# Kernel optimization log

Hardware: AMD Instinct MI355X
Metric: run time of the kernel (lower is better)

The kernel has to match this reference:

```python
import jax, jax.numpy as jnp
import numpy as np
from jax import lax

V = 33          # n_vertices
B, H, W = 8, 1024, 1024
RES = 256       # backbone input resolution
N_FEATS = 128 * 8 * 8  # 8192


def setup_inputs() -> dict:
    key = jax.random.key(0)
    ks = jax.random.split(key, 16)
    inp = {"x": jax.random.uniform(ks[0], (B, 3, H, W), jnp.float32)}
    chans = [(3, 16), (16, 32), (32, 64), (64, 128), (128, 128)]
    for i, (ci, co) in enumerate(chans):
        inp[f"cw{i}"] = jax.random.normal(ks[1 + i], (co, ci, 3, 3), jnp.float32) / float(np.sqrt(ci * 9))
        inp[f"cb{i}"] = jnp.zeros((co,), jnp.float32)
    for i, c in enumerate([16, 32, 64, 128]):
        inp[f"g{i}"] = 1.0 + 0.02 * jax.random.normal(ks[6 + i], (c,), jnp.float32)  # InstanceNorm affine init
        inp[f"be{i}"] = jnp.zeros((c,), jnp.float32)
    inp["wg_w"] = 0.01 * jax.random.normal(ks[10], (3, N_FEATS), jnp.float32)
    inp["wg_b"] = jnp.ones((3,), jnp.float32)  # init_weights: ones bias
    # basis LUT bank: rank 0 = identity LUT (meshgrid, flip(0)), other ranks small noise
    grid = jnp.stack(jnp.meshgrid(*[jnp.arange(V, dtype=jnp.float32)] * 3, indexing="ij"), 0) / (V - 1)
    identity = jnp.flip(grid, 0).reshape(1, -1)          # [1, 3*V^3]
    rest = 0.01 * jax.random.normal(ks[11], (2, 3 * V ** 3), jnp.float32)
    inp["lut_w"] = jnp.concatenate([identity, rest], 0).T  # [3*V^3, n_ranks]
    inp["vertices"] = jnp.broadcast_to(jnp.arange(V, dtype=jnp.float32) / (V - 1), (3, V))[None]  # [1,3,V]
    return inp


def _conv(x, w, b, stride=2):
    y = lax.conv_general_dilated(x, w, (stride, stride), ((1, 1), (1, 1)),
                                 dimension_numbers=("NCHW", "OIHW", "NCHW"))
    return y + b[None, :, None, None]


def _inorm(x, g, be, eps=1e-5):
    m = x.mean((2, 3), keepdims=True)
    v = x.var((2, 3), keepdims=True)  # biased, matches torch InstanceNorm
    return (x - m) / jnp.sqrt(v + eps) * g[None, :, None, None] + be[None, :, None, None]


def _leaky(x):
    return jnp.where(x >= 0, x, 0.2 * x)


def _backbone(x, cws, cbs, gs, bes):
    h = jax.image.resize(x, (x.shape[0], 3, RES, RES), "bilinear")
    for i in range(4):  # Conv -> LeakyReLU -> InstanceNorm
        h = _inorm(_leaky(_conv(h, cws[i], cbs[i])), gs[i], bes[i])
    h = _leaky(_conv(h, cws[4], cbs[4]))  # last block, no norm; dropout = identity (eval)
    return h.reshape(x.shape[0], -1)


def _ailut(img, luts, vertices):
    # img [B,3,H,W], luts [B,3,V,V,V] (axes: out_ch, b, g, r), vertices [1,3,V]
    Bn, Vn = img.shape[0], vertices.shape[-1]
    verts = jnp.broadcast_to(vertices, (Bn, 3, Vn))
    q = img.reshape(Bn * 3, -1)
    vflat = verts.reshape(Bn * 3, Vn)
    idx = jax.vmap(lambda v, qq: jnp.searchsorted(v, qq, side="right"))(vflat, q) - 1
    idx = jnp.clip(idx, 0, Vn - 2).reshape(Bn, 3, -1)       # bin index per (b, color, pixel)
    lo = jnp.take_along_axis(verts, idx, axis=2)
    hi = jnp.take_along_axis(verts, idx + 1, axis=2)
    d = (img.reshape(Bn, 3, -1) - lo) / (hi - lo)           # fractional offset
    ir, ig, ib = idx[:, 0], idx[:, 1], idx[:, 2]
    dr, dg, db = d[:, 0], d[:, 1], d[:, 2]
    lflat = luts.reshape(Bn, 3, Vn ** 3)
    out = jnp.zeros_like(d)
    for ob in (0, 1):
        for og in (0, 1):
            for orr in (0, 1):
                w = ((db if ob else 1 - db) * (dg if og else 1 - dg) * (dr if orr else 1 - dr))
                lin = ((ib + ob) * Vn + (ig + og)) * Vn + (ir + orr)
                vals = jnp.take_along_axis(lflat, lin[:, None, :], axis=2)  # [B,3,N]
                out = out + w[:, None, :] * vals
    return out.reshape(img.shape)


def reference(x, cw0, cw1, cw2, cw3, cw4, cb0, cb1, cb2, cb3, cb4,
              g0, g1, g2, g3, be0, be1, be2, be3, wg_w, wg_b, lut_w, vertices):
    codes = _backbone(x, [cw0, cw1, cw2, cw3, cw4], [cb0, cb1, cb2, cb3, cb4],
                      [g0, g1, g2, g3], [be0, be1, be2, be3])   # [B, 8192]
    weights = codes @ wg_w.T + wg_b                              # [B, 3]
    luts = (weights @ lut_w.T).reshape(x.shape[0], 3, V, V, V)   # [B,3,V,V,V]
    outs = _ailut(x, luts, vertices)
    return outs, weights, luts, vertices
```

## Files before the change

kernel.cpp:

```cpp
#include <hip/hip_runtime.h>
#include <hip/hip_bf16.h>
#include <stdint.h>

typedef unsigned int U32;

static __device__ __forceinline__ U32 f2bf_rne(float f){
  U32 u; __builtin_memcpy(&u, &f, 4);
  u = (u + 0x7fffu + ((u >> 16) & 1u)) >> 16;
  return u & 0xffffu;
}
static __device__ __forceinline__ float bflo2f(U32 p){
  U32 u = p << 16; float f; __builtin_memcpy(&f, &u, 4); return f;
}
static __device__ __forceinline__ float bfhi2f(U32 p){
  U32 u = p & 0xffff0000u; float f; __builtin_memcpy(&f, &u, 4); return f;
}

__global__ void resize_k(const float* __restrict__ x, float* __restrict__ resz){
  __shared__ float hs[68][64];
  int blk = blockIdx.x;
  int tx = blk & 3;
  int ty = (blk >> 2) & 15;
  int bc = blk >> 6;
  int ox0 = tx << 6, oy0 = ty << 4;
  int r0 = 4*oy0 - 2; if (r0 < 0) r0 = 0;
  if (r0 > 956) r0 = 958;
  const float* src = x + ((size_t)bc << 20);
  #pragma unroll 4
  for (int i = threadIdx.x; i < 68*64; i += 256){
    int r   = i >> 6;
    int oxl = i & 63;
    int ox  = ox0 + oxl;
    int rr  = r0 + r; if (rr > 1023) rr = 1023;
    const float2* row2 = (const float2*)(src + ((size_t)rr << 10));
    float acc;
    if (ox >= 1 && ox <= 254){
      float2 a = row2[2*ox-1];
      float2 b = row2[2*ox];
      float2 c = row2[2*ox+1];
      float2 d = row2[2*ox+2];
      acc = (1.f/32)*(a.x + d.y)
          + (3.f/32)*(a.y + d.x)
          + (5.f/32)*(b.x + c.y)
          + (7.f/32)*(b.y + c.x);
    } else if (ox == 0){
      float2 a = row2[0], b = row2[1], c = row2[2];
      acc = (0.625f/3.5f)*a.x + (0.875f/3.5f)*a.y
          + (0.875f/3.5f)*b.x + (0.625f/3.5f)*b.y
          + (0.375f/3.5f)*c.x + (0.125f/3.5f)*c.y;
    } else {
      float2 a = row2[509], b = row2[510], c = row2[511];
      acc = (0.125f/3.5f)*a.x + (0.375f/3.5f)*a.y
          + (0.625f/3.5f)*b.x + (0.875f/3.5f)*b.y
          + (0.875f/3.5f)*c.x + (0.625f/3.5f)*c.y;
    }
    hs[r][oxl] = acc;
  }
  __syncthreads();
  for (int i = threadIdx.x; i < 16*64; i += 256){
    int oyl = i >> 6, oxl = i & 63;
    int oy = oy0 + oyl;
    float acc;
    if (oy >= 1 && oy <= 254){
      int j0 = 4*oy - 2 - r0;
      acc = (1.f/32)*(hs[j0+0][oxl] + hs[j0+7][oxl])
          + (3.f/32)*(hs[j0+1][oxl] + hs[j0+6][oxl])
          + (5.f/32)*(hs[j0+2][oxl] + hs[j0+5][oxl])
          + (7.f/32)*(hs[j0+3][oxl] + hs[j0+4][oxl]);
    } else if (oy == 0){
      acc = (0.625f/3.5f)*hs[0][oxl] + (0.875f/3.5f)*hs[1][oxl]
          + (0.875f/3.5f)*hs[2][oxl] + (0.625f/3.5f)*hs[3][oxl]
          + (0.375f/3.5f)*hs[4][oxl] + (0.125f/3.5f)*hs[5][oxl];
    } else {
      int j0 = 1018 - r0;
      acc = (0.125f/3.5f)*hs[j0+0][oxl] + (0.375f/3.5f)*hs[j0+1][oxl]
          + (0.625f/3.5f)*hs[j0+2][oxl] + (0.875f/3.5f)*hs[j0+3][oxl]
          + (0.875f/3.5f)*hs[j0+4][oxl] + (0.625f/3.5f)*hs[j0+5][oxl];
    }
    resz[((size_t)bc << 16) + ((size_t)oy << 8) + (size_t)(ox0 + oxl)] = acc;
  }
}

__global__ void conv0_k(const float* __restrict__ in, const float* __restrict__ w,
                        const float* __restrict__ bias, float* __restrict__ out,
                        float* __restrict__ st0){
  __shared__ float tile[3][5][264];
  __shared__ float wsm[432];
  __shared__ float bs[16];
  __shared__ float sred[4][16][2];
  int t = blockIdx.x & 63;
  int b = blockIdx.x >> 6;
  for (int i = threadIdx.x; i < 432; i += 256) wsm[i] = w[i];
  if (threadIdx.x < 16) bs[threadIdx.x] = bias[threadIdx.x];
  const float* inb = in + (size_t)b*3*65536;
  int ih0 = 4*t - 1;
  for (int i = threadIdx.x; i < 3*5*258; i += 256){
    int ci  = i / (5*258);
    int rem = i % (5*258);
    int r   = rem / 258;
    int cc  = rem % 258;
    int ih  = ih0 + r;
    int iw  = cc - 1;
    float v = 0.f;
    if ((unsigned)ih < 256u && (unsigned)iw < 256u)
      v = inb[ci*65536 + ih*256 + iw];
    tile[ci][r][cc] = v;
  }
  __syncthreads();
  int lr = threadIdx.x >> 7;
  int ow = threadIdx.x & 127;
  float acc[16];
  #pragma unroll
  for (int j = 0; j < 16; j++) acc[j] = 0.f;
  #pragma unroll
  for (int ci = 0; ci < 3; ci++)
    #pragma unroll
    for (int kh = 0; kh < 3; kh++)
      #pragma unroll
      for (int kw = 0; kw < 3; kw++){
        float v = tile[ci][2*lr + kh][2*ow + kw];
        #pragma unroll
        for (int j = 0; j < 16; j++)
          acc[j] += v * wsm[j*27 + ci*9 + kh*3 + kw];
      }
  int s = t*256 + (int)threadIdx.x;
  size_t obase = (size_t)b*16*16384 + (size_t)s;
  float av[16];
  #pragma unroll
  for (int j = 0; j < 16; j++){
    float a = acc[j] + bs[j];
    a = (a >= 0.f) ? a : 0.2f*a;
    av[j] = a;
    out[obase + (size_t)j*16384] = a;
  }
  int wv = threadIdx.x >> 6;
  #pragma unroll
  for (int j = 0; j < 16; j++){
    float s1 = av[j], s2 = av[j]*av[j];
    #pragma unroll
    for (int o = 32; o > 0; o >>= 1){ s1 += __shfl_down(s1, o, 64); s2 += __shfl_down(s2, o, 64); }
    if ((threadIdx.x & 63) == 0){ sred[wv][j][0] = s1; sred[wv][j][1] = s2; }
  }
  __syncthreads();
  if (threadIdx.x < 16){
    float s1 = 0.f, s2 = 0.f;
    #pragma unroll
    for (int w2 = 0; w2 < 4; w2++){ s1 += sred[w2][threadIdx.x][0]; s2 += sred[w2][threadIdx.x][1]; }
    float* e = st0 + (((size_t)b*16 + threadIdx.x)*64 + t)*2;
    e[0] = s1; e[1] = s2;
  }
}

template<int CI, int CO, int IN, int OUT, int COB, int SPLIT, int TIN, int TOUT>
__global__ void __launch_bounds__(256, 1)
conv_leaky_k(const float* __restrict__ in, const float* __restrict__ w,
             const float* __restrict__ bias, float* __restrict__ out,
             const float* __restrict__ st_in, const float* __restrict__ g,
             const float* __restrict__ be, float* __restrict__ st_out){
  constexpr int P     = 256 / SPLIT;
  constexpr int TILES = (OUT*OUT + P - 1) / P;
  constexpr int NCB   = CO / COB;
  constexpr int CIS   = CI / SPLIT;
  constexpr int SUBS  = (TIN > 0) ? ((256/CI < TIN) ? 256/CI : TIN) : 1;
  int blk  = blockIdx.x;
  int b    = blk & 7;
  int rest = blk >> 3;
  int tile = rest % TILES;
  int cob  = rest / TILES;
  int co0  = cob * COB;
  __shared__ float ws[COB * CI * 9];
  __shared__ float bs[COB];
  __shared__ float red[(SPLIT > 1) ? 256 * COB : 1];
  __shared__ float sc[(TIN > 0) ? CI : 1];
  __shared__ float sh[(TIN > 0) ? CI : 1];
  __shared__ float pre[(TIN > 0) ? CI : 1][SUBS][2];
  for (int i = threadIdx.x; i < COB*CI*9; i += 256) ws[i] = w[(size_t)co0*CI*9 + i];
  if (threadIdx.x < COB) bs[threadIdx.x] = bias[co0 + threadIdx.x];
  if constexpr (TIN > 0){
    int c = threadIdx.x / SUBS, sub = threadIdx.x % SUBS;
    if (c < CI){
      const float* e = st_in + ((size_t)b*CI + c)*TIN*2;
      float s1 = 0.f, s2 = 0.f;
      for (int t2 = sub; t2 < TIN; t2 += SUBS){ s1 += e[t2*2]; s2 += e[t2*2+1]; }
      pre[c][sub][0] = s1; pre[c][sub][1] = s2;
    }
  }
  __syncthreads();
  if constexpr (TIN > 0){
    if (threadIdx.x < CI){
      float s1 = 0.f, s2 = 0.f;
      #pragma unroll
      for (int t2 = 0; t2 < SUBS; t2++){ s1 += pre[threadIdx.x][t2][0]; s2 += pre[threadIdx.x][t2][1]; }
      constexpr float hw = (float)(IN*IN);
      float mean = s1 * (1.f/hw);
      float var  = s2 * (1.f/hw) - mean*mean;
      float rstd = 1.f / sqrtf(var + 1e-5f);
      float scv  = g[threadIdx.x] * rstd;
      sc[threadIdx.x] = scv;
      sh[threadIdx.x] = be[threadIdx.x] - mean*scv;
    }
  }
  __syncthreads();
  int pix = threadIdx.x % P;
  int sp  = threadIdx.x / P;
  int s   = tile*P + pix;
  int oh = s / OUT, ow = s % OUT;
  float acc[COB];
  #pragma unroll
  for (int j = 0; j < COB; j++) acc[j] = 0.f;
  const float* inb = in + ((size_t)b*CI + sp*CIS) * (IN*IN);
  #pragma unroll
  for (int c0 = 0; c0 < CIS; c0 += 4){
    constexpr int CH = (CIS < 4) ? CIS : 4;
    #pragma unroll
    for (int kh = 0; kh < 3; kh++){
      int ih = oh*2 - 1 + kh;
      if ((unsigned)ih >= (unsigned)IN) continue;
      #pragma unroll
      for (int kw = 0; kw < 3; kw++){
        int iw = ow*2 - 1 + kw;
        if ((unsigned)iw >= (unsigned)IN) continue;
        const float* p0 = inb + (size_t)c0*(IN*IN) + ih*IN + iw;
        float vv[CH];
        #pragma unroll
        for (int ci = 0; ci < CH; ci++) vv[ci] = p0[(size_t)ci*(IN*IN)];
        if constexpr (TIN > 0){
          #pragma unroll
          for (int ci = 0; ci < CH; ci++) vv[ci] = vv[ci]*sc[sp*CIS+c0+ci] + sh[sp*CIS+c0+ci];
        }
        #pragma unroll
        for (int ci = 0; ci < CH; ci++){
          #pragma unroll
          for (int j = 0; j < COB; j++)
            acc[j] += vv[ci] * ws[j*CI*9 + (sp*CIS+c0+ci)*9 + kh*3 + kw];
        }
      }
    }
  }
  if constexpr (SPLIT > 1){
    #pragma unroll
    for (int j = 0; j < COB; j++) red[threadIdx.x*COB + j] = acc[j];
    __syncthreads();
    if (sp == 0){
      #pragma unroll
      for (int s2 = 1; s2 < SPLIT; s2++)
        #pragma unroll
        for (int j = 0; j < COB; j++)
          acc[j] += red[(pix + s2*P)*COB + j];
    }
  }
  float av[COB];
  if (sp == 0){
    size_t obase = ((size_t)b*CO + co0) * (size_t)(OUT*OUT) + s;
    #pragma unroll
    for (int j = 0; j < COB; j++){
      float a = acc[j] + bs[j];
      a = (a >= 0.f) ? a : 0.2f*a;
      av[j] = a;
      out[obase + (size_t)j*OUT*OUT] = a;
    }
  }
  if constexpr (TOUT > 0){
    constexpr int NW = P / 64;
    __shared__ float sred2[NW][COB][2];
    if (threadIdx.x < P){
      #pragma unroll
      for (int j = 0; j < COB; j++){
        float s1 = av[j], s2 = av[j]*av[j];
        #pragma unroll
        for (int o = 32; o > 0; o >>= 1){ s1 += __shfl_down(s1, o, 64); s2 += __shfl_down(s2, o, 64); }
        if ((threadIdx.x & 63) == 0){ int wv = threadIdx.x >> 6; sred2[wv][j][0] = s1; sred2[wv][j][1] = s2; }
      }
    }
    __syncthreads();
    if (threadIdx.x < COB){
      float s1 = 0.f, s2 = 0.f;
      #pragma unroll
      for (int wv = 0; wv < NW; wv++){ s1 += sred2[wv][threadIdx.x][0]; s2 += sred2[wv][threadIdx.x][1]; }
      float* e = st_out + (((size_t)b*CO + co0 + threadIdx.x)*TOUT + tile)*2;
      e[0] = s1; e[1] = s2;
    }
  }
}

static __device__ __forceinline__ float blockReduceSum256(float v, float* red){
  #pragma unroll
  for (int o = 32; o > 0; o >>= 1) v += __shfl_down(v, o, 64);
  __syncthreads();
  if ((threadIdx.x & 63) == 0) red[threadIdx.x >> 6] = v;
  __syncthreads();
  return red[0] + red[1] + red[2] + red[3];
}

__global__ void gemv_w_k(const float* __restrict__ codes, const float* __restrict__ wg_w,
                         const float* __restrict__ wg_b, float* __restrict__ wf,
                         float* __restrict__ outp){
  __shared__ float red[4];
  int b = blockIdx.x / 3, o = blockIdx.x % 3;
  const float* cp = codes + (size_t)b*8192;
  const float* wp = wg_w + (size_t)o*8192;
  float s = 0.f;
  for (int i = threadIdx.x; i < 8192; i += 256) s += cp[i] * wp[i];
  float tot = blockReduceSum256(s, red);
  if (threadIdx.x == 0){
    float v = tot + wg_b[o];
    wf[blockIdx.x] = v;
    outp[25165824 + blockIdx.x] = v;
  }
}

__global__ void luts_k(const float* __restrict__ wf, const float* __restrict__ lut_w,
                       const float* __restrict__ verts, U32* __restrict__ lp,
                       float* __restrict__ outp){
  int j = blockIdx.x * 256 + threadIdx.x;
  if (blockIdx.x == 0 && threadIdx.x < 99) outp[26028336 + threadIdx.x] = verts[threadIdx.x];
  if (j >= 107811) return;
  int jn = (j + 1 < 107811) ? (j + 1) : j;
  float l0 = lut_w[3*j+0], l1 = lut_w[3*j+1], l2 = lut_w[3*j+2];
  float m0 = lut_w[3*jn+0], m1 = lut_w[3*jn+1], m2 = lut_w[3*jn+2];
  int c = j / 35937;
  int i = j - c * 35937;
  #pragma unroll
  for (int b = 0; b < 8; b++){
    float w0 = wf[b*3+0], w1 = wf[b*3+1], w2 = wf[b*3+2];
    float v  = w0*l0 + w1*l1 + w2*l2;
    float vn = w0*m0 + w1*m1 + w2*m2;
    outp[25165848 + (size_t)b*107811 + j] = v;
    lp[(size_t)(b*3 + c)*35940 + i] = f2bf_rne(v) | (f2bf_rne(vn) << 16);
  }
}

static __device__ __forceinline__ void apply_phase(const U32* ls, const float4* rv,
                                                   const float4* gv, const float4* bv,
                                                   float* ob, int base){
  #pragma unroll
  for (int k = 0; k < 4; k++){
    float rr[4] = {rv[k].x, rv[k].y, rv[k].z, rv[k].w};
    float gg[4] = {gv[k].x, gv[k].y, gv[k].z, gv[k].w};
    float bb[4] = {bv[k].x, bv[k].y, bv[k].z, bv[k].w};
    U32 pw[4][4];
    float w00[4], w01[4], w10[4], w11[4], drx[4];
    #pragma unroll
    for (int h = 0; h < 4; h++){
      float rq = rr[h] * 32.f;
      float gq = gg[h] * 32.f;
      float bq = bb[h] * 32.f;
      int ir = (int)rq; ir = ir > 31 ? 31 : ir;
      int ig = (int)gq; ig = ig > 31 ? 31 : ig;
      int ib = (int)bq; ib = ib > 31 ? 31 : ib;
      float dr = rq - (float)ir;
      float dg = gq - (float)ig;
      float db = bq - (float)ib;
      int lin = (ib*33 + ig)*33 + ir;
      pw[h][0] = ls[lin];
      pw[h][1] = ls[lin+33];
      pw[h][2] = ls[lin+1089];
      pw[h][3] = ls[lin+1122];
      float t = db*dg;
      w11[h] = t;
      w10[h] = db - t;
      w01[h] = dg - t;
      w00[h] = 1.f - db - dg + t;
      drx[h] = dr;
    }
    float res[4];
    #pragma unroll
    for (int h = 0; h < 4; h++){
      float odr = 1.f - drx[h];
      float v0 = odr*bflo2f(pw[h][0]) + drx[h]*bfhi2f(pw[h][0]);
      float v1 = odr*bflo2f(pw[h][1]) + drx[h]*bfhi2f(pw[h][1]);
      float v2 = odr*bflo2f(pw[h][2]) + drx[h]*bfhi2f(pw[h][2]);
      float v3 = odr*bflo2f(pw[h][3]) + drx[h]*bfhi2f(pw[h][3]);
      res[h] = w00[h]*v0 + w01[h]*v1 + w10[h]*v2 + w11[h]*v3;
    }
    *(float4*)(ob + base + k*4096) = make_float4(res[0], res[1], res[2], res[3]);
  }
}

__global__ void __launch_bounds__(1024, 4) ailut_apply_k(const float* __restrict__ x,
                                                         const U32* __restrict__ lp,
                                                         float* __restrict__ outp){
  __shared__ U32 ls[35936];
  int b = blockIdx.z, c = blockIdx.y;
  const size_t plane = 1048576;
  const float* xb = x + (size_t)b*3*plane;
  int base = blockIdx.x * 32768 + (int)threadIdx.x*4;
  float4 rv[4], gv[4], bv[4];
  #pragma unroll
  for (int k = 0; k < 4; k++){
    int p0 = base + k*4096;
    rv[k] = *(const float4*)(xb + p0);
    gv[k] = *(const float4*)(xb + plane + p0);
    bv[k] = *(const float4*)(xb + 2*plane + p0);
  }
  const U32* lsrc = lp + (size_t)(b*3 + c)*35940;
  for (int i = threadIdx.x; i < 8984; i += 1024)
    __builtin_amdgcn_global_load_lds(
        (const __attribute__((address_space(1))) void*)(lsrc + 4*(size_t)i),
        (__attribute__((address_space(3))) void*)(ls + 4*i), 16, 0, 0);
  __syncthreads();
  float* ob = outp + ((size_t)b*3 + c)*plane;
  apply_phase(ls, rv, gv, bv, ob, base);
  #pragma unroll
  for (int k = 0; k < 4; k++){
    int p0 = base + 16384 + k*4096;
    rv[k] = *(const float4*)(xb + p0);
    gv[k] = *(const float4*)(xb + plane + p0);
    bv[k] = *(const float4*)(xb + 2*plane + p0);
  }
  apply_phase(ls, rv, gv, bv, ob, base + 16384);
}

extern "C" void kernel_launch(void* const* d_in, const int* in_sizes, int n_in,
                              void* d_out, int out_size, void* d_ws, size_t ws_size,
                              hipStream_t stream){
  const float* x    = (const float*)d_in[0];
  const float* cw0  = (const float*)d_in[1];
  const float* cb0  = (const float*)d_in[2];
  const float* cw1  = (const float*)d_in[3];
  const float* cb1  = (const float*)d_in[4];
  const float* cw2  = (const float*)d_in[5];
  const float* cb2  = (const float*)d_in[6];
  const float* cw3  = (const float*)d_in[7];
  const float* cb3  = (const float*)d_in[8];
  const float* cw4  = (const float*)d_in[9];
  const float* cb4  = (const float*)d_in[10];
  const float* g0   = (const float*)d_in[11];
  const float* be0  = (const float*)d_in[12];
  const float* g1   = (const float*)d_in[13];
  const float* be1  = (const float*)d_in[14];
  const float* g2   = (const float*)d_in[15];
  const float* be2  = (const float*)d_in[16];
  const float* g3   = (const float*)d_in[17];
  const float* be3  = (const float*)d_in[18];
  const float* wgw  = (const float*)d_in[19];
  const float* wgb  = (const float*)d_in[20];
  const float* lutw = (const float*)d_in[21];
  const float* vert = (const float*)d_in[22];
  float* out = (float*)d_out;
  float* ws  = (float*)d_ws;

  U32*   lp   = (U32*)ws;
  float* wf   = ws + 862592;
  float* st0  = ws + 862720;
  float* st1  = ws + 879104;
  float* st2  = ws + 887296;
  float* st3  = ws + 891392;
  float* resz = ws + 895488;
  float* act0 = ws + 2468352;
  float* act1 = act0 + 2097152;
  float* act2 = act1 + 1048576;
  float* act3 = act2 + 524288;
  float* act4 = act3 + 262144;

  resize_k<<<1536, 256, 0, stream>>>(x, resz);

  conv0_k<<<512, 256, 0, stream>>>(resz, cw0, cb0, act0, st0);
  conv_leaky_k<16,32,128,64,8,1,64,16>
      <<<8*4*16, 256, 0, stream>>>(act0, cw1, cb1, act1, st0, g0, be0, st1);
  conv_leaky_k<32,64,64,32,4,1,16,4>
      <<<8*16*4, 256, 0, stream>>>(act1, cw2, cb2, act2, st1, g1, be1, st2);
  conv_leaky_k<64,128,32,16,4,2,4,2>
      <<<8*32*2, 256, 0, stream>>>(act2, cw3, cb3, act3, st2, g2, be2, st3);
  conv_leaky_k<128,128,16,8,4,4,2,0>
      <<<8*32*1, 256, 0, stream>>>(act3, cw4, cb4, act4, st3, g3, be3, nullptr);

  gemv_w_k<<<24, 256, 0, stream>>>(act4, wgw, wgb, wf, out);
  luts_k<<<422, 256, 0, stream>>>(wf, lutw, vert, lp, out);
  ailut_apply_k<<<dim3(32,3,8), 1024, 0, stream>>>(x, lp, out);
}
```

Measured before the change: 193.1 us.

## Fuse last conv with weight-generator GEMV and fold reduction into LUT kernel

The final conv+LeakyReLU layer becomes a dedicated kernel that immediately multiplies its activations by the weight-generator matrix and writes per-block partial sums, so the 8192-wide code vector is never stored. The separate GEMV launch is removed, and the LUT generation kernel now sums the 32 partials per batch plus the bias in shared memory. This drops one kernel launch and a global round trip. In exchange, every LUT block redundantly recomputes the tiny reduction and the summation order changes.

```diff
diff --git a/kernel.cpp b/kernel.cpp
--- a/kernel.cpp
+++ b/kernel.cpp
@@ -159,7 +159,6 @@
              const float* __restrict__ be, float* __restrict__ st_out){
   constexpr int P     = 256 / SPLIT;
   constexpr int TILES = (OUT*OUT + P - 1) / P;
-  constexpr int NCB   = CO / COB;
   constexpr int CIS   = CI / SPLIT;
   constexpr int SUBS  = (TIN > 0) ? ((256/CI < TIN) ? 256/CI : TIN) : 1;
   int blk  = blockIdx.x;
@@ -283,37 +282,122 @@
   }
 }
 
-static __device__ __forceinline__ float blockReduceSum256(float v, float* red){
-  #pragma unroll
-  for (int o = 32; o > 0; o >>= 1) v += __shfl_down(v, o, 64);
-  __syncthreads();
-  if ((threadIdx.x & 63) == 0) red[threadIdx.x >> 6] = v;
-  __syncthreads();
-  return red[0] + red[1] + red[2] + red[3];
-}
-
-__global__ void gemv_w_k(const float* __restrict__ codes, const float* __restrict__ wg_w,
-                         const float* __restrict__ wg_b, float* __restrict__ wf,
-                         float* __restrict__ outp){
-  __shared__ float red[4];
-  int b = blockIdx.x / 3, o = blockIdx.x % 3;
-  const float* cp = codes + (size_t)b*8192;
-  const float* wp = wg_w + (size_t)o*8192;
-  float s = 0.f;
-  for (int i = threadIdx.x; i < 8192; i += 256) s += cp[i] * wp[i];
-  float tot = blockReduceSum256(s, red);
-  if (threadIdx.x == 0){
-    float v = tot + wg_b[o];
-    wf[blockIdx.x] = v;
-    outp[25165824 + blockIdx.x] = v;
-  }
-}
-
-__global__ void luts_k(const float* __restrict__ wf, const float* __restrict__ lut_w,
-                       const float* __restrict__ verts, U32* __restrict__ lp,
-                       float* __restrict__ outp){
+__global__ void __launch_bounds__(256, 1)
+conv4_gemv_k(const float* __restrict__ in, const float* __restrict__ w,
+             const float* __restrict__ bias, const float* __restrict__ st_in,
+             const float* __restrict__ g, const float* __restrict__ be,
+             const float* __restrict__ wgw, float* __restrict__ part){
+  __shared__ float ws[4*128*9];
+  __shared__ float bs[4];
+  __shared__ float red[256*4];
+  __shared__ float sc[128], sh[128];
+  __shared__ float pre[128][2][2];
+  int blk = blockIdx.x;
+  int b   = blk & 7;
+  int cob = blk >> 3;
+  int co0 = cob * 4;
+  for (int i = threadIdx.x; i < 4*128*9; i += 256) ws[i] = w[(size_t)co0*128*9 + i];
+  if (threadIdx.x < 4) bs[threadIdx.x] = bias[co0 + threadIdx.x];
+  {
+    int c = threadIdx.x >> 1, sub = threadIdx.x & 1;
+    if (c < 128){
+      const float* e = st_in + ((size_t)b*128 + c)*2*2;
+      pre[c][sub][0] = e[sub*2]; pre[c][sub][1] = e[sub*2+1];
+    }
+  }
+  __syncthreads();
+  if (threadIdx.x < 128){
+    float s1 = pre[threadIdx.x][0][0] + pre[threadIdx.x][1][0];
+    float s2 = pre[threadIdx.x][0][1] + pre[threadIdx.x][1][1];
+    float mean = s1 * (1.f/256.f);
+    float var  = s2 * (1.f/256.f) - mean*mean;
+    float rstd = 1.f / sqrtf(var + 1e-5f);
+    float scv  = g[threadIdx.x] * rstd;
+    sc[threadIdx.x] = scv;
+    sh[threadIdx.x] = be[threadIdx.x] - mean*scv;
+  }
+  __syncthreads();
+  int pix = threadIdx.x & 63;
+  int sp  = threadIdx.x >> 6;
+  int s   = pix;
+  int oh = s >> 3, ow = s & 7;
+  float acc[4];
+  #pragma unroll
+  for (int j = 0; j < 4; j++) acc[j] = 0.f;
+  const float* inb = in + ((size_t)b*128 + sp*32) * 256;
+  #pragma unroll
+  for (int c0 = 0; c0 < 32; c0 += 4){
+    #pragma unroll
+    for (int kh = 0; kh < 3; kh++){
+      int ih = oh*2 - 1 + kh;
+      if ((unsigned)ih >= 16u) continue;
+      #pragma unroll
+      for (int kw = 0; kw < 3; kw++){
+        int iw = ow*2 - 1 + kw;
+        if ((unsigned)iw >= 16u) continue;
+        const float* p0 = inb + (size_t)c0*256 + ih*16 + iw;
+        float vv[4];
+        #pragma unroll
+        for (int ci = 0; ci < 4; ci++) vv[ci] = p0[ci*256];
+        #pragma unroll
+        for (int ci = 0; ci < 4; ci++) vv[ci] = vv[ci]*sc[sp*32+c0+ci] + sh[sp*32+c0+ci];
+        #pragma unroll
+        for (int ci = 0; ci < 4; ci++){
+          #pragma unroll
+          for (int j = 0; j < 4; j++)
+            acc[j] += vv[ci] * ws[j*128*9 + (sp*32+c0+ci)*9 + kh*3 + kw];
+        }
+      }
+    }
+  }
+  #pragma unroll
+  for (int j = 0; j < 4; j++) red[threadIdx.x*4 + j] = acc[j];
+  __syncthreads();
+  if (sp == 0){
+    #pragma unroll
+    for (int s2 = 1; s2 < 4; s2++)
+      #pragma unroll
+      for (int j = 0; j < 4; j++)
+        acc[j] += red[(pix + s2*64)*4 + j];
+    float av[4];
+    #pragma unroll
+    for (int j = 0; j < 4; j++){
+      float a = acc[j] + bs[j];
+      av[j] = (a >= 0.f) ? a : 0.2f*a;
+    }
+    float p3[3];
+    #pragma unroll
+    for (int o = 0; o < 3; o++){
+      float t = 0.f;
+      #pragma unroll
+      for (int j = 0; j < 4; j++)
+        t += av[j] * wgw[(size_t)o*8192 + (size_t)(co0+j)*64 + s];
+      #pragma unroll
+      for (int off = 32; off > 0; off >>= 1) t += __shfl_down(t, off, 64);
+      p3[o] = t;
+    }
+    if (pix == 0){
+      float* e = part + ((size_t)b*32 + cob)*3;
+      e[0] = p3[0]; e[1] = p3[1]; e[2] = p3[2];
+    }
+  }
+}
+
+__global__ void luts_k(const float* __restrict__ part, const float* __restrict__ wgb,
+                       const float* __restrict__ lut_w, const float* __restrict__ verts,
+                       U32* __restrict__ lp, float* __restrict__ outp){
+  __shared__ float wf_s[24];
+  if (threadIdx.x < 24){
+    int b = threadIdx.x / 3, o = threadIdx.x % 3;
+    float s = 0.f;
+    for (int cob = 0; cob < 32; cob++) s += part[((size_t)b*32 + cob)*3 + o];
+    s += wgb[o];
+    wf_s[threadIdx.x] = s;
+    if (blockIdx.x == 0) outp[25165824 + threadIdx.x] = s;
+  }
+  __syncthreads();
+  if (blockIdx.x == 0 && threadIdx.x < 99) outp[26028336 + threadIdx.x] = verts[threadIdx.x];
   int j = blockIdx.x * 256 + threadIdx.x;
-  if (blockIdx.x == 0 && threadIdx.x < 99) outp[26028336 + threadIdx.x] = verts[threadIdx.x];
   if (j >= 107811) return;
   int jn = (j + 1 < 107811) ? (j + 1) : j;
   float l0 = lut_w[3*j+0], l1 = lut_w[3*j+1], l2 = lut_w[3*j+2];
@@ -322,7 +406,7 @@
   int i = j - c * 35937;
   #pragma unroll
   for (int b = 0; b < 8; b++){
-    float w0 = wf[b*3+0], w1 = wf[b*3+1], w2 = wf[b*3+2];
+    float w0 = wf_s[b*3+0], w1 = wf_s[b*3+1], w2 = wf_s[b*3+2];
     float v  = w0*l0 + w1*l1 + w2*l2;
     float vn = w0*m0 + w1*m1 + w2*m2;
     outp[25165848 + (size_t)b*107811 + j] = v;
@@ -441,7 +525,6 @@
   float* ws  = (float*)d_ws;
 
   U32*   lp   = (U32*)ws;
-  float* wf   = ws + 862592;
   float* st0  = ws + 862720;
   float* st1  = ws + 879104;
   float* st2  = ws + 887296;
@@ -451,7 +534,7 @@
   float* act1 = act0 + 2097152;
   float* act2 = act1 + 1048576;
   float* act3 = act2 + 524288;
-  float* act4 = act3 + 262144;
+  float* part = act3 + 262144;
 
   resize_k<<<1536, 256, 0, stream>>>(x, resz);
 
@@ -462,10 +545,8 @@
       <<<8*16*4, 256, 0, stream>>>(act1, cw2, cb2, act2, st1, g1, be1, st2);
   conv_leaky_k<64,128,32,16,4,2,4,2>
       <<<8*32*2, 256, 0, stream>>>(act2, cw3, cb3, act3, st2, g2, be2, st3);
-  conv_leaky_k<128,128,16,8,4,4,2,0>
-      <<<8*32*1, 256, 0, stream>>>(act3, cw4, cb4, act4, st3, g3, be3, nullptr);
-
-  gemv_w_k<<<24, 256, 0, stream>>>(act4, wgw, wgb, wf, out);
-  luts_k<<<422, 256, 0, stream>>>(wf, lutw, vert, lp, out);
+  conv4_gemv_k<<<256, 256, 0, stream>>>(act3, cw4, cb4, st3, g3, be3, wgw, part);
+
+  luts_k<<<422, 256, 0, stream>>>(part, wgb, lutw, vert, lp, out);
   ailut_apply_k<<<dim3(32,3,8), 1024, 0, stream>>>(x, lp, out);
 }
```

New measurement: 182.6 us (median of 2 runs). 5.4% less time.
